# Optimization experiments

Hardware: AMD Instinct MI355X
Metric: run time of the kernel (lower is better)

## Reference

```python
import jax, jax.numpy as jnp
import numpy as np

# Module hyperparameters (from init_kwargs)
P = 96                 # num_of_patches
W = 1536.0             # input width
H = 1536.0             # input height
XPS = W / P            # x patch size = 16
YPS = H / P            # y patch size = 16
PROB_THR = 0.9
IOU_THR = 0.5
N = P * P              # total candidate boxes


def setup_inputs() -> dict:
    key = jax.random.key(0)
    # x: [5, P, P] -> channel 0 = probability, 1..4 = (x, y, w, h) in [0,1)
    x = jax.random.uniform(key, (5, P, P), dtype=jnp.float32)
    return {"x": x}


def _pairwise_iou(b):
    # b: [N, 4] xyxy
    x1, y1, x2, y2 = b[:, 0], b[:, 1], b[:, 2], b[:, 3]
    area = (x2 - x1) * (y2 - y1)                       # [N]
    ix1 = jnp.maximum(x1[:, None], x1[None, :])
    iy1 = jnp.maximum(y1[:, None], y1[None, :])
    ix2 = jnp.minimum(x2[:, None], x2[None, :])
    iy2 = jnp.minimum(y2[:, None], y2[None, :])
    inter = jnp.clip(ix2 - ix1, 0.0) * jnp.clip(iy2 - iy1, 0.0)
    union = area[:, None] + area[None, :] - inter
    return jnp.where(union > 0, inter / union, 0.0)    # [N, N]


def _forward(x):
    # --- scale_batch_bbx_xywh, applied densely (invalid entries are masked later) ---
    p = x[0]
    ii = jnp.arange(P, dtype=x.dtype)[:, None]   # row index i
    jj = jnp.arange(P, dtype=x.dtype)[None, :]   # col index j
    bx = x[1] * XPS + ii * XPS
    by = x[2] * YPS + jj * YPS
    bw = x[3] * W
    bh = x[4] * H
    bbx = jnp.stack([p, bx, by, bw, bh], axis=0).reshape(5, N).T   # [N, 5] (p, x, y, w, h)

    # --- remove_low_probability_bbx: fixed-shape validity mask instead of filtering ---
    scores = bbx[:, 0]
    valid = scores > PROB_THR

    # --- convert_batch_to_xyxy + round ---
    x1 = jnp.round(bbx[:, 1])
    y1 = jnp.round(bbx[:, 2])
    x2 = jnp.round(bbx[:, 3] + bbx[:, 1])
    y2 = jnp.round(bbx[:, 4] + bbx[:, 2])

    # --- greedy NMS (torchvision semantics): sort by score desc, suppress by IoU ---
    sort_key = jnp.where(valid, scores, -jnp.inf)
    order = jnp.argsort(-sort_key)
    boxes = jnp.stack([x1, y1, x2, y2], axis=1)[order]   # [N, 4] sorted
    sc = scores[order]
    v = valid[order]
    iou = _pairwise_iou(boxes)                           # [N, N]

    def body(kept, i):
        suppressed = jnp.any(kept & (iou[i] > IOU_THR))
        ki = v[i] & ~suppressed
        return kept.at[i].set(ki), ki

    _, keeps = jax.lax.scan(body, jnp.zeros((N,), bool), jnp.arange(N))

    # --- cat([scores, bbx]) then convert_batch_to_xywh on kept rows ---
    out = jnp.stack(
        [sc, boxes[:, 0], boxes[:, 1], boxes[:, 2] - boxes[:, 0], boxes[:, 3] - boxes[:, 1]],
        axis=1,
    )  # [N, 5] = (score, x, y, w, h), score-descending order like nms output
    out = jnp.where(keeps[:, None], out, 0.0)
    return out, keeps


def reference(x):
    # Returns (out [N,5], keep_mask [N]); rows with keep_mask=False are zeroed.
    # This is the fixed-shape equivalent of the variable-length torch output.
    return _forward(x)
```

## Files before the change

kernel.cpp:

```cpp
#include <hip/hip_runtime.h>

#define PP 96
#define NB (PP*PP)
#define NCH (NB/64)
#define PROB_THR 0.9f
#define FAST_CAP 1024
#define LSTRIDE 1034

typedef unsigned long long u64;
typedef unsigned int u32;

__device__ __forceinline__ void decode_core(int n, float xv, float yv, float wv, float hv,
                                            float& X1, float& Y1, float& X2, float& Y2)
{
    int i = n / PP;
    int j = n - i * PP;
    float bx = __fadd_rn(__fmul_rn(xv, 16.0f), (float)i * 16.0f);
    float by = __fadd_rn(__fmul_rn(yv, 16.0f), (float)j * 16.0f);
    float bw = __fmul_rn(wv, 1536.0f);
    float bh = __fmul_rn(hv, 1536.0f);
    X1 = rintf(bx);
    Y1 = rintf(by);
    X2 = rintf(__fadd_rn(bw, bx));
    Y2 = rintf(__fadd_rn(bh, by));
}

__device__ __forceinline__ void decode_box(const float* __restrict__ x, int n,
                                           float& X1, float& Y1, float& X2, float& Y2)
{
    decode_core(n, x[NB + n], x[2 * NB + n], x[3 * NB + n], x[4 * NB + n], X1, Y1, X2, Y2);
}

__device__ __forceinline__ int iou_hit_nodiv(float ix1, float iy1, float ix2, float iy2, float iar,
                                             float jx1, float jy1, float jx2, float jy2, float jar)
{
    float xx1 = fmaxf(ix1, jx1), yy1 = fmaxf(iy1, jy1);
    float xx2 = fminf(ix2, jx2), yy2 = fminf(iy2, jy2);
    float iw = fmaxf(__fsub_rn(xx2, xx1), 0.0f);
    float ih = fmaxf(__fsub_rn(yy2, yy1), 0.0f);
    float inter = __fmul_rn(iw, ih);
    float uni = __fsub_rn(__fadd_rn(iar, jar), inter);
    return (uni > 0.0f && __fadd_rn(inter, inter) > uni) ? 1 : 0;
}

__device__ __forceinline__ int iou_hit_div(float ix1, float iy1, float ix2, float iy2, float iar,
                                           float jx1, float jy1, float jx2, float jy2, float jar)
{
    float xx1 = fmaxf(ix1, jx1), yy1 = fmaxf(iy1, jy1);
    float xx2 = fminf(ix2, jx2), yy2 = fminf(iy2, jy2);
    float iw = fmaxf(__fsub_rn(xx2, xx1), 0.0f);
    float ih = fmaxf(__fsub_rn(yy2, yy1), 0.0f);
    float inter = __fmul_rn(iw, ih);
    float uni = __fsub_rn(__fadd_rn(iar, jar), inter);
    return (uni > 0.0f && __fdiv_rn(inter, uni) > 0.5f) ? 1 : 0;
}

__global__ void __launch_bounds__(256) k_sort(
    const float* __restrict__ x,
    float* __restrict__ gss, float4* __restrict__ gbox,
    u64* __restrict__ skeys, int* __restrict__ counter, int ws_ok)
{
    __shared__ u64 lmask[NCH];
    __shared__ int pc[NCH], loff[NCH];
    __shared__ int sM;
    __shared__ u64 kdb[FAST_CAP];
    __shared__ int prank[256];

    const int tid = threadIdx.x;
    const int lane = tid & 63;
    const int wv = tid >> 6;
    const int b = blockIdx.x;

    #pragma unroll
    for (int g = 0; g < 36; g += 6) {
        float sv[6];
        #pragma unroll
        for (int u = 0; u < 6; ++u)
            sv[u] = x[((wv * 36 + g + u) << 6) + lane];
        #pragma unroll
        for (int u = 0; u < 6; ++u) {
            u64 m = __ballot(sv[u] > PROB_THR);
            if (lane == 0) lmask[wv * 36 + g + u] = m;
        }
    }
    __syncthreads();
    if (tid < NCH) pc[tid] = __popcll(lmask[tid]);
    __syncthreads();
    if (tid < 64) {
        int acc = 0;
        for (int seg = 0; seg < 3; ++seg) {
            int c = (seg << 6) + lane;
            int pv = (c < NCH) ? pc[c] : 0;
            int v = pv;
            #pragma unroll
            for (int off = 1; off < 64; off <<= 1) {
                int u = __shfl_up(v, off);
                if (lane >= off) v += u;
            }
            if (c < NCH) loff[c] = acc + v - pv;
            acc += __shfl(v, 63);
        }
        if (lane == 0) sM = acc;
    }
    __syncthreads();
    const int M = sM;
    const bool fast = (M <= FAST_CAP) && ws_ok;
    if (b == 0 && tid == 0) counter[0] = M;

    if (!fast) {
        if (b == 0) {
            for (int c = wv; c < NCH; c += 4) {
                float s = x[(c << 6) + lane];
                u64 m = lmask[c];
                if ((m >> lane) & 1ull) {
                    int pos = loff[c] + __popcll(m & ((1ull << lane) - 1ull));
                    int n = (c << 6) + lane;
                    skeys[pos] = ((u64)__float_as_uint(s) << 32) | (u64)(NB - 1 - n);
                }
            }
        }
        return;
    }

    for (int c = wv; c < NCH; c += 4) {
        float s = x[(c << 6) + lane];
        u64 m = lmask[c];
        if ((m >> lane) & 1ull) {
            int pos = loff[c] + __popcll(m & ((1ull << lane) - 1ull));
            int n = (c << 6) + lane;
            kdb[pos] = ((u64)__float_as_uint(s) << 32) | (u64)(NB - 1 - n);
        }
    }
    for (int q = M + tid; q < FAST_CAP; q += 256) kdb[q] = 0ull;
    __syncthreads();

    const int cand = (b << 6) + lane;
    const u64 k0 = kdb[cand];
    const int n0 = NB - 1 - (int)(k0 & 0xFFFFFFFFull);
    float xv0 = x[NB + n0], yv0 = x[2 * NB + n0];
    float wv0 = x[3 * NB + n0], hv0 = x[4 * NB + n0];
    int r = 0;
    const int nck = (M + 63) >> 6;
    for (int ch = wv; ch < nck; ch += 4) {
        u64 kq = kdb[(ch << 6) + lane];
        u32 qlo = (u32)kq, qhi = (u32)(kq >> 32);
        #pragma unroll
        for (int i = 0; i < 64; ++i) {
            u32 blo = (u32)__builtin_amdgcn_readlane((int)qlo, i);
            u32 bhi = (u32)__builtin_amdgcn_readlane((int)qhi, i);
            u64 kb = ((u64)bhi << 32) | (u64)blo;
            r += (kb > k0) ? 1 : 0;
        }
    }
    prank[tid] = r;
    __syncthreads();
    if (tid < 64 && cand < M) {
        int rk = prank[tid] + prank[64 + tid] + prank[128 + tid] + prank[192 + tid];
        float X1, Y1, X2, Y2;
        decode_core(n0, xv0, yv0, wv0, hv0, X1, Y1, X2, Y2);
        gbox[rk] = make_float4(X1, Y1, X2, Y2);
        gss[rk] = __uint_as_float((u32)(k0 >> 32));
    }
}

__global__ void __launch_bounds__(256) k_adj(
    float* __restrict__ out, const float4* __restrict__ gbox,
    const int* __restrict__ counter, u64* __restrict__ adjT, int ws_ok)
{
    __shared__ float4 lb[FAST_CAP];
    __shared__ float la[FAST_CAP];
    int M = counter[0]; if (M > NB) M = NB;
    const int tid = threadIdx.x, lane = tid & 63, wv = tid >> 6, b = blockIdx.x;

    float4 z4 = make_float4(0.f, 0.f, 0.f, 0.f);
    for (int q = tid; q < 216; q += 256)
        ((float4*)out)[b * 216 + q] = z4;

    const bool fast = (M <= FAST_CAP) && ws_ok;
    if (!fast) return;
    if ((b << 4) >= M) return;

    const int W = (M + 63) >> 6;
    for (int f = tid; f < M; f += 256) {
        float4 bb = gbox[f];
        lb[f] = bb;
        la[f] = __fmul_rn(__fsub_rn(bb.z, bb.x), __fsub_rn(bb.w, bb.y));
    }
    __syncthreads();

    #pragma unroll
    for (int r = 0; r < 4; ++r) {
        int i = (b << 4) + (r << 2) + wv;
        if (i >= M) break;
        float4 bi = lb[i];
        float iar = la[i];
        for (int kk = 0; kk < W; ++kk) {
            int j = (kk << 6) + lane;
            float4 bj = lb[j & (FAST_CAP - 1)];
            float jar = la[j & (FAST_CAP - 1)];
            int hit = (j < M) && iou_hit_nodiv(bi.x, bi.y, bi.z, bi.w, iar,
                                               bj.x, bj.y, bj.z, bj.w, jar);
            u64 mm = __ballot(hit);
            if (lane == 0) adjT[((size_t)kk << 10) + i] = mm;
        }
    }
}

__global__ void __launch_bounds__(1024) k_sweep(
    const float* __restrict__ x, float* __restrict__ out,
    float* __restrict__ gss, float4* __restrict__ gbox,
    const u64* __restrict__ skeys, const int* __restrict__ counter,
    const u64* __restrict__ adjT, int ws_ok)
{
    __shared__ __align__(16) u64 Lds[16 * LSTRIDE];
    __shared__ u64 keepw[NCH];
    int M = counter[0]; if (M > NB) M = NB;
    const int W = (M + 63) >> 6;
    const bool fast = (M <= FAST_CAP) && ws_ok;
    const int tid = threadIdx.x, lane = tid & 63;

    if (fast) {
        const int npair = W << 9;
        const ulonglong2* gp = (const ulonglong2*)adjT;
        ulonglong2 v[8];
        #pragma unroll
        for (int u = 0; u < 8; ++u) {
            int f = tid + (u << 10);
            v[u] = (f < npair) ? gp[f] : make_ulonglong2(0ull, 0ull);
        }
        #pragma unroll
        for (int u = 0; u < 8; ++u) {
            int f = tid + (u << 10);
            if (f < npair) {
                int w = f >> 9, r2 = f & 511;
                ((ulonglong2*)Lds)[w * (LSTRIDE >> 1) + r2] = v[u];
            }
        }
        __syncthreads();

        if (tid < 64) {
            const int wl = (lane < W) ? lane : 0;
            u32 supl = 0u, suph = 0u, dl = 0u, dh = 0u;
            u64 mykw = 0ull;
            const int nrb = (M + 31) >> 5;
            for (int rb = 0; rb < nrb; ++rb) {
                const int c = rb >> 1;
                const int base = rb << 5;
                const u64* crow = Lds + (size_t)c * LSTRIDE + base;
                const u64* rrow = Lds + (size_t)wl * LSTRIDE + base;
                if (!(rb & 1)) {
                    if (rb == 0) { dl = 0u; dh = 0u; }
                    else { dl = (u32)__shfl((int)supl, c); dh = (u32)__shfl((int)suph, c); }
                    int rem = M - (c << 6);
                    if (rem < 64) {
                        if (rem >= 32) dh |= 0xFFFFFFFFu << (rem - 32);
                        else { dh = 0xFFFFFFFFu; dl |= 0xFFFFFFFFu << rem; }
                    }
                }
                u64 colb[32];
                #pragma unroll
                for (int q = 0; q < 16; ++q) {
                    ulonglong2 t2 = ((const ulonglong2*)crow)[q];
                    colb[2 * q] = t2.x; colb[2 * q + 1] = t2.y;
                }
                u32 kw = 0u;
                if (!(rb & 1)) {
                    #pragma unroll
                    for (int t = 0; t < 32; ++t) {
                        u32 bbit = (dl >> t) & 1u;
                        u32 m = bbit - 1u;
                        dl |= (u32)colb[t] & m;
                        dh |= (u32)(colb[t] >> 32) & m;
                        kw |= m & (1u << t);
                    }
                } else {
                    #pragma unroll
                    for (int t = 0; t < 32; ++t) {
                        u32 bbit = (dh >> t) & 1u;
                        u32 m = bbit - 1u;
                        dl |= (u32)colb[t] & m;
                        dh |= (u32)(colb[t] >> 32) & m;
                        kw |= m & (1u << t);
                    }
                }
                u32 bits = kw;
                while (bits) {
                    int t = __builtin_ctz(bits);
                    bits &= bits - 1u;
                    u64 rv = rrow[t];
                    supl |= (u32)rv;
                    suph |= (u32)(rv >> 32);
                }
                mykw |= (lane == c) ? ((u64)kw << ((rb & 1) << 5)) : 0ull;
            }
            keepw[lane] = mykw;
        }
    } else {
        for (int t = tid; t < M; t += 1024) {
            u64 key = skeys[t];
            int r = 0;
            for (int q = 0; q < M; ++q) r += (skeys[q] > key) ? 1 : 0;
            int n = NB - 1 - (int)(key & 0xFFFFFFFFull);
            float X1, Y1, X2, Y2;
            decode_box(x, n, X1, Y1, X2, Y2);
            gbox[r] = make_float4(X1, Y1, X2, Y2);
            gss[r] = __uint_as_float((u32)(key >> 32));
        }
        __threadfence();
        __syncthreads();
        if (tid < 64) {
            u64 kbs[3] = {0ull, 0ull, 0ull};
            for (int i = 0; i < M; ++i) {
                float4 bi = gbox[i];
                float iar = __fmul_rn(__fsub_rn(bi.z, bi.x), __fsub_rn(bi.w, bi.y));
                int hit = 0;
                int nk = (i > lane) ? ((i - lane + 63) >> 6) : 0;
                for (int w = 0; w < 3 && !hit; ++w) {
                    int klim = nk - (w << 6);
                    if (klim <= 0) break;
                    u64 bits = kbs[w];
                    if (klim < 64) bits &= ((1ull << klim) - 1ull);
                    while (bits) {
                        int kk2 = __builtin_ctzll(bits);
                        bits &= bits - 1ull;
                        int jj = lane + (((w << 6) + kk2) << 6);
                        float4 bj = gbox[jj];
                        float jar = __fmul_rn(__fsub_rn(bj.z, bj.x), __fsub_rn(bj.w, bj.y));
                        if (iou_hit_div(bi.x, bi.y, bi.z, bi.w, iar,
                                        bj.x, bj.y, bj.z, bj.w, jar)) { hit = 1; break; }
                    }
                }
                int suppressed = __any(hit);
                if (!suppressed && lane == (i & 63)) kbs[(i >> 6) >> 6] |= 1ull << ((i >> 6) & 63);
            }
            int NWrd = (M + 63) >> 6;
            for (int wd = 0; wd < NWrd; ++wd) {
                u64 bit = (kbs[wd >> 6] >> (wd & 63)) & 1ull;
                u64 word = __ballot(bit != 0);
                if (lane == 0 && wd < NCH) keepw[wd] = word;
            }
        }
    }
    __syncthreads();

    for (int i = tid; i < M; i += 1024) {
        if ((keepw[i >> 6] >> (i & 63)) & 1ull) {
            float4 bb = gbox[i];
            out[i * 5 + 0] = gss[i];
            out[i * 5 + 1] = bb.x;
            out[i * 5 + 2] = bb.y;
            out[i * 5 + 3] = __fsub_rn(bb.z, bb.x);
            out[i * 5 + 4] = __fsub_rn(bb.w, bb.y);
            out[5 * NB + i] = 1.0f;
        }
    }
}

extern "C" void kernel_launch(void* const* d_in, const int* in_sizes, int n_in,
                              void* d_out, int out_size, void* d_ws, size_t ws_size,
                              hipStream_t stream) {
    const float* x = (const float*)d_in[0];
    float* out = (float*)d_out;

    char* ws = (char*)d_ws;
    int* counter = (int*)ws;
    float*  gss  = (float*)(ws + 16);
    float4* gbox = (float4*)(ws + 16 + (size_t)4 * NB);
    u64*    adjT = (u64*)(ws + 16 + (size_t)4 * NB + (size_t)16 * NB);
    u64*    skeys = (u64*)((char*)adjT + (size_t)16384 * 8);
    const size_t NEEDED = 16 + (size_t)4 * NB + (size_t)16 * NB
                        + (size_t)16384 * 8 + (size_t)8 * NB;
    int ws_ok = (ws_size >= NEEDED) ? 1 : 0;

    k_sort<<<16, 256, 0, stream>>>(x, gss, gbox, skeys, counter, ws_ok);
    k_adj<<<64, 256, 0, stream>>>(out, gbox, counter, adjT, ws_ok);
    k_sweep<<<1, 1024, 0, stream>>>(x, out, gss, gbox, skeys, counter, adjT, ws_ok);
}
```

Baseline: 112.3 us.

## Shrink sweep block to 256 threads and make suppression OR branchless

```diff
diff --git a/kernel.cpp b/kernel.cpp
--- a/kernel.cpp
+++ b/kernel.cpp
@@ -206,7 +206,7 @@
     }
 }
 
-__global__ void __launch_bounds__(1024) k_sweep(
+__global__ void __launch_bounds__(256) k_sweep(
     const float* __restrict__ x, float* __restrict__ out,
     float* __restrict__ gss, float4* __restrict__ gbox,
     const u64* __restrict__ skeys, const int* __restrict__ counter,
@@ -222,18 +222,21 @@
     if (fast) {
         const int npair = W << 9;
         const ulonglong2* gp = (const ulonglong2*)adjT;
-        ulonglong2 v[8];
-        #pragma unroll
-        for (int u = 0; u < 8; ++u) {
-            int f = tid + (u << 10);
-            v[u] = (f < npair) ? gp[f] : make_ulonglong2(0ull, 0ull);
-        }
-        #pragma unroll
-        for (int u = 0; u < 8; ++u) {
-            int f = tid + (u << 10);
-            if (f < npair) {
-                int w = f >> 9, r2 = f & 511;
-                ((ulonglong2*)Lds)[w * (LSTRIDE >> 1) + r2] = v[u];
+        for (int r = 0; r < 4; ++r) {
+            int fb = (r << 11) + tid;
+            ulonglong2 v[8];
+            #pragma unroll
+            for (int u = 0; u < 8; ++u) {
+                int f = fb + (u << 8);
+                v[u] = (f < npair) ? gp[f] : make_ulonglong2(0ull, 0ull);
+            }
+            #pragma unroll
+            for (int u = 0; u < 8; ++u) {
+                int f = fb + (u << 8);
+                if (f < npair) {
+                    int w = f >> 9, r2 = f & 511;
+                    ((ulonglong2*)Lds)[w * (LSTRIDE >> 1) + r2] = v[u];
+                }
             }
         }
         __syncthreads();
@@ -246,8 +249,19 @@
             for (int rb = 0; rb < nrb; ++rb) {
                 const int c = rb >> 1;
                 const int base = rb << 5;
-                const u64* crow = Lds + (size_t)c * LSTRIDE + base;
-                const u64* rrow = Lds + (size_t)wl * LSTRIDE + base;
+                const ulonglong2* crow = (const ulonglong2*)(Lds + (size_t)c * LSTRIDE + base);
+                const ulonglong2* rrow = (const ulonglong2*)(Lds + (size_t)wl * LSTRIDE + base);
+                u64 colb[32], rowb[32];
+                #pragma unroll
+                for (int q = 0; q < 16; ++q) {
+                    ulonglong2 t2 = crow[q];
+                    colb[2 * q] = t2.x; colb[2 * q + 1] = t2.y;
+                }
+                #pragma unroll
+                for (int q = 0; q < 16; ++q) {
+                    ulonglong2 t2 = rrow[q];
+                    rowb[2 * q] = t2.x; rowb[2 * q + 1] = t2.y;
+                }
                 if (!(rb & 1)) {
                     if (rb == 0) { dl = 0u; dh = 0u; }
                     else { dl = (u32)__shfl((int)supl, c); dh = (u32)__shfl((int)suph, c); }
@@ -256,12 +270,6 @@
                         if (rem >= 32) dh |= 0xFFFFFFFFu << (rem - 32);
                         else { dh = 0xFFFFFFFFu; dl |= 0xFFFFFFFFu << rem; }
                     }
-                }
-                u64 colb[32];
-                #pragma unroll
-                for (int q = 0; q < 16; ++q) {
-                    ulonglong2 t2 = ((const ulonglong2*)crow)[q];
-                    colb[2 * q] = t2.x; colb[2 * q + 1] = t2.y;
                 }
                 u32 kw = 0u;
                 if (!(rb & 1)) {
@@ -283,20 +291,18 @@
                         kw |= m & (1u << t);
                     }
                 }
-                u32 bits = kw;
-                while (bits) {
-                    int t = __builtin_ctz(bits);
-                    bits &= bits - 1u;
-                    u64 rv = rrow[t];
-                    supl |= (u32)rv;
-                    suph |= (u32)(rv >> 32);
+                #pragma unroll
+                for (int t = 0; t < 32; ++t) {
+                    u32 m = 0u - ((kw >> t) & 1u);
+                    supl |= (u32)rowb[t] & m;
+                    suph |= (u32)(rowb[t] >> 32) & m;
                 }
                 mykw |= (lane == c) ? ((u64)kw << ((rb & 1) << 5)) : 0ull;
             }
             keepw[lane] = mykw;
         }
     } else {
-        for (int t = tid; t < M; t += 1024) {
+        for (int t = tid; t < M; t += 256) {
             u64 key = skeys[t];
             int r = 0;
             for (int q = 0; q < M; ++q) r += (skeys[q] > key) ? 1 : 0;
@@ -343,7 +349,7 @@
     }
     __syncthreads();
 
-    for (int i = tid; i < M; i += 1024) {
+    for (int i = tid; i < M; i += 256) {
         if ((keepw[i >> 6] >> (i & 63)) & 1ull) {
             float4 bb = gbox[i];
             out[i * 5 + 0] = gss[i];
@@ -374,5 +380,5 @@
 
     k_sort<<<16, 256, 0, stream>>>(x, gss, gbox, skeys, counter, ws_ok);
     k_adj<<<64, 256, 0, stream>>>(out, gbox, counter, adjT, ws_ok);
-    k_sweep<<<1, 1024, 0, stream>>>(x, out, gss, gbox, skeys, counter, adjT, ws_ok);
-}
+    k_sweep<<<1, 256, 0, stream>>>(x, out, gss, gbox, skeys, counter, adjT, ws_ok);
+}
```

Result: faster. 103.5 us (-7.8%).
